# Performance work log

Hardware: AMD Instinct MI355X
Metric: run time of the kernel (lower is better)

The kernel has to match this reference:

```python
import jax, jax.numpy as jnp
import numpy as np
import math

B, L, D = 2, 1024, 1024
H, DK, DV = 8, 1536, 1536
DEPTH = 1
R = math.exp(4 - 2 * DEPTH) / (math.exp(4 - 2 * DEPTH) + 1)
TEMP = DK ** 0.5
LN_EPS = 1e-5


def setup_inputs() -> dict:
    key = jax.random.key(0)
    ks = jax.random.split(key, 16)
    s = 0.02
    return {
        "q": jax.random.normal(ks[0], (B, L, D), jnp.float32),
        "k": jax.random.normal(ks[1], (B, L, D), jnp.float32),
        "v": jax.random.normal(ks[2], (B, L, D), jnp.float32),
        "mask": jax.random.randint(ks[3], (B, L, 1), 0, 2, jnp.int32),
        "w_qs_w": jax.random.normal(ks[4], (H * DK, D), jnp.float32) * s,
        "w_qs_b": jnp.zeros((H * DK,), jnp.float32),
        "w_ks_w": jax.random.normal(ks[5], (H * DK, D), jnp.float32) * s,
        "w_ks_b": jnp.zeros((H * DK,), jnp.float32),
        "w_vs_w": jax.random.normal(ks[6], (H * DV, D), jnp.float32) * s,
        "w_vs_b": jnp.zeros((H * DV,), jnp.float32),
        "fc_w": jax.random.normal(ks[7], (D, H * DV), jnp.float32) * s,
        "ln_scale": jnp.ones((D,), jnp.float32),
        "ln_bias": jnp.zeros((D,), jnp.float32),
    }


def reference(q, k, v, mask, w_qs_w, w_qs_b, w_ks_w, w_ks_b, w_vs_w, w_vs_b, fc_w, ln_scale, ln_bias):
    Bq, Lq, _ = q.shape
    Lk = k.shape[1]
    residual = q
    # QKV projections, split into heads, flatten as (batch, head)
    qh = (q @ w_qs_w.T + w_qs_b).reshape(Bq, Lq, H, DK).transpose(0, 2, 1, 3).reshape(Bq * H, Lq, DK)
    kh = (k @ w_ks_w.T + w_ks_b).reshape(Bq, Lk, H, DK).transpose(0, 2, 1, 3).reshape(Bq * H, Lk, DK)
    vh = (v @ w_vs_w.T + w_vs_b).reshape(Bq, Lk, H, DV).transpose(0, 2, 1, 3).reshape(Bq * H, Lk, DV)
    # mask: repeat(n_head,1,1) -> (head, batch) ordering, exactly as original
    maskf = mask.astype(jnp.float32)
    mask_rep = jnp.tile(maskf, (H, 1, 1))  # [H*B, Lq, 1]
    maskb = mask_rep != 0
    atten = jnp.einsum('bqd,bkd->bqk', qh / TEMP, kh)  # [B*H, Lq, Lk]
    atten = jnp.where(maskb, 1e-9, atten)  # masked_fill_(mask.bool(), 1e-9)
    new_mask = (1.0 - R) * maskb.astype(jnp.float32) + R * mask_rep  # [B*H, Lq, 1]
    atten = jax.nn.softmax(atten, axis=-1) * new_mask
    out = jnp.einsum('bqk,bkd->bqd', atten, vh)
    out = out.reshape(Bq, H, Lq, DV).transpose(0, 2, 1, 3).reshape(Bq, Lq, H * DV)
    out = out @ fc_w.T
    x = out + residual
    mu = jnp.mean(x, axis=-1, keepdims=True)
    var = jnp.mean((x - mu) ** 2, axis=-1, keepdims=True)
    out = (x - mu) / jnp.sqrt(var + LN_EPS) * ln_scale + ln_bias
    return (out, atten)
```

## Files before the change

### kernel.cpp

```cpp
#include <hip/hip_runtime.h>
#include <hip/hip_bf16.h>

#define B_   2
#define L_   1024
#define D_   1024
#define H_   8
#define DV_  1536
#define HDV_ 12288
#define INV_L (1.0f/1024.0f)


__global__ void __launch_bounds__(256) k1(const float* __restrict__ v,
                                          float* __restrict__ vsum,
                                          const int* __restrict__ mask,
                                          float* __restrict__ atten) {
    int bx = blockIdx.x, t = threadIdx.x;
    if (bx < 32) {
        __shared__ float4 lds[16][16];
        int b  = bx >> 4;
        int s  = bx & 15;
        int c4 = t & 15;
        int rg = t >> 4;
        const float4* vp = (const float4*)(v + (size_t)b * L_ * D_)
                           + (size_t)s * 16 + c4;
        float4 acc = make_float4(0.f, 0.f, 0.f, 0.f);
        #pragma unroll 8
        for (int r = 0; r < 64; ++r) {
            float4 x = vp[(size_t)(rg * 64 + r) * (D_ / 4)];
            acc.x += x.x; acc.y += x.y; acc.z += x.z; acc.w += x.w;
        }
        lds[rg][c4] = acc;
        __syncthreads();
        if (t < 16) {
            float4 a = make_float4(0.f, 0.f, 0.f, 0.f);
            #pragma unroll
            for (int g = 0; g < 16; ++g) {
                float4 x = lds[g][t];
                a.x += x.x; a.y += x.y; a.z += x.z; a.w += x.w;
            }
            ((float4*)(vsum + (size_t)b * D_ + (size_t)s * 64))[t] = a;
        }
    } else {
        int r0 = (bx - 32) * 8;
        #pragma unroll
        for (int rr = 0; rr < 8; ++rr) {
            int r  = r0 + rr;
            int i  = r >> 10;
            int qi = r & 1023;
            float val = (mask[((i & 1) << 10) + qi] != 0) ? INV_L : 0.f;
            ((float4*)(atten + (size_t)r * L_))[t] = make_float4(val, val, val, val);
        }
    }
}

__global__ void __launch_bounds__(256) k_vproj(const float* __restrict__ vsum,
                                               const float* __restrict__ wv,
                                               const float* __restrict__ bv,
                                               float* __restrict__ S) {
    int gid  = blockIdx.x * 256 + threadIdx.x;
    int m    = gid >> 6;
    int lane = threadIdx.x & 63;
    const float4* row = (const float4*)(wv + (size_t)m * D_);
    const float4* v0  = (const float4*)vsum;
    const float4* v1  = (const float4*)(vsum + D_);
    float a0 = 0.f, a1 = 0.f;
    #pragma unroll
    for (int it = 0; it < 4; ++it) {
        int c = it * 64 + lane;
        float4 w4 = row[c];
        float4 s0 = v0[c];
        float4 s1 = v1[c];
        a0 += w4.x*s0.x + w4.y*s0.y + w4.z*s0.z + w4.w*s0.w;
        a1 += w4.x*s1.x + w4.y*s1.y + w4.z*s1.z + w4.w*s1.w;
    }
    #pragma unroll
    for (int off = 32; off; off >>= 1) {
        a0 += __shfl_down(a0, off);
        a1 += __shfl_down(a1, off);
    }
    if (lane == 0) {
        float bb = bv[m] * (float)L_;
        S[m]        = a0 + bb;
        S[HDV_ + m] = a1 + bb;
    }
}

__global__ void __launch_bounds__(256) k_fc(const float* __restrict__ S,
                                            const float* __restrict__ fcw,
                                            float* __restrict__ G) {
    __shared__ float red[16];
    int j = blockIdx.x, t = threadIdx.x;
    const float4* row = (const float4*)(fcw + (size_t)j * HDV_);
    const float4* S0  = (const float4*)S;
    const float4* S1  = (const float4*)(S + HDV_);
    float g00 = 0.f, g01 = 0.f, g10 = 0.f, g11 = 0.f;
    #pragma unroll
    for (int it = 0; it < 12; ++it) {
        int t4 = it * 256 + t;
        int p  = (t4 / 384) & 1;
        float4 w4 = row[t4];
        float4 s0 = S0[t4];
        float4 s1 = S1[t4];
        float d0 = w4.x*s0.x + w4.y*s0.y + w4.z*s0.z + w4.w*s0.w;
        float d1 = w4.x*s1.x + w4.y*s1.y + w4.z*s1.z + w4.w*s1.w;
        if (p) { g01 += d0; g11 += d1; } else { g00 += d0; g10 += d1; }
    }
    #pragma unroll
    for (int off = 32; off; off >>= 1) {
        g00 += __shfl_down(g00, off);
        g01 += __shfl_down(g01, off);
        g10 += __shfl_down(g10, off);
        g11 += __shfl_down(g11, off);
    }
    int lane = t & 63, w = t >> 6;
    if (lane == 0) {
        red[w * 4 + 0] = g00; red[w * 4 + 1] = g01;
        red[w * 4 + 2] = g10; red[w * 4 + 3] = g11;
    }
    __syncthreads();
    if (t < 4) {
        float x = red[t] + red[4 + t] + red[8 + t] + red[12 + t];
        G[(size_t)t * D_ + j] = x;
    }
}

__global__ void __launch_bounds__(256) k_ln(const float* __restrict__ qin,
                                            const int* __restrict__ mask,
                                            const float* __restrict__ G,
                                            const float* __restrict__ lns,
                                            const float* __restrict__ lnb,
                                            float* __restrict__ out) {
    __shared__ float red[8];
    int row = blockIdx.x;
    int b   = row >> 10;
    int qi  = row & 1023;
    float m0 = (mask[qi]      != 0) ? INV_L : 0.f;
    float m1 = (mask[L_ + qi] != 0) ? INV_L : 0.f;
    const float4* q4 = (const float4*)(qin + (size_t)row * D_);
    const float4* g0 = (const float4*)(G + (size_t)(2 * b) * D_);
    const float4* g1 = (const float4*)(G + (size_t)(2 * b + 1) * D_);
    int t = threadIdx.x;
    float4 a = q4[t], u = g0[t], w = g1[t];
    float4 x;
    x.x = a.x + m0 * u.x + m1 * w.x;
    x.y = a.y + m0 * u.y + m1 * w.y;
    x.z = a.z + m0 * u.z + m1 * w.z;
    x.w = a.w + m0 * u.w + m1 * w.w;
    float s  = x.x + x.y + x.z + x.w;
    float ss = x.x*x.x + x.y*x.y + x.z*x.z + x.w*x.w;
    #pragma unroll
    for (int off = 32; off; off >>= 1) {
        s  += __shfl_down(s, off);
        ss += __shfl_down(ss, off);
    }
    int lane = t & 63, wv = t >> 6;
    if (lane == 0) { red[wv] = s; red[4 + wv] = ss; }
    __syncthreads();
    if (t == 0) {
        float sAll  = red[0] + red[1] + red[2] + red[3];
        float ssAll = red[4] + red[5] + red[6] + red[7];
        float mu  = sAll * INV_L;
        float var = ssAll * INV_L - mu * mu;
        red[0] = mu;
        red[1] = rsqrtf(var + 1e-5f);
    }
    __syncthreads();
    float mu = red[0], inv = red[1];
    float4 sc = ((const float4*)lns)[t];
    float4 bi = ((const float4*)lnb)[t];
    float4 o;
    o.x = (x.x - mu) * inv * sc.x + bi.x;
    o.y = (x.y - mu) * inv * sc.y + bi.y;
    o.z = (x.z - mu) * inv * sc.z + bi.z;
    o.w = (x.w - mu) * inv * sc.w + bi.w;
    ((float4*)(out + (size_t)row * D_))[t] = o;
}

extern "C" void kernel_launch(void* const* d_in, const int* in_sizes, int n_in,
                              void* d_out, int out_size, void* d_ws, size_t ws_size,
                              hipStream_t stream) {
    const float* q    = (const float*)d_in[0];
    const float* v    = (const float*)d_in[2];
    const int*   mask = (const int*)d_in[3];
    const float* wv   = (const float*)d_in[8];
    const float* bv   = (const float*)d_in[9];
    const float* fcw  = (const float*)d_in[10];
    const float* lns  = (const float*)d_in[11];
    const float* lnb  = (const float*)d_in[12];

    float* out   = (float*)d_out;
    float* atten = out + (size_t)B_ * L_ * D_;

    float* ws   = (float*)d_ws;
    float* vsum = ws;
    float* S    = ws + 2048;
    float* G    = ws + 26624;

    k1      <<<32 + 2048, 256, 0, stream>>>(v, vsum, mask, atten);
    k_vproj <<<(HDV_ * 64) / 256, 256, 0, stream>>>(vsum, wv, bv, S);
    k_fc    <<<D_, 256, 0, stream>>>(S, fcw, G);
    k_ln    <<<B_ * L_, 256, 0, stream>>>(q, mask, G, lns, lnb, out);
}
```

Baseline: 41.70 us.

## Spread atten fill writes across vproj and fc kernels to overlap bandwidth

```diff
diff --git a/kernel.cpp b/kernel.cpp
--- a/kernel.cpp
+++ b/kernel.cpp
@@ -9,6 +9,19 @@
 #define HDV_ 12288
 #define INV_L (1.0f/1024.0f)
 
+
+__device__ __forceinline__ void atten_rows8(const int* __restrict__ mask,
+                                            float* __restrict__ atten,
+                                            int r0, int t) {
+    #pragma unroll
+    for (int rr = 0; rr < 8; ++rr) {
+        int r  = r0 + rr;
+        int i  = r >> 10;
+        int qi = r & 1023;
+        float val = (mask[((i & 1) << 10) + qi] != 0) ? INV_L : 0.f;
+        ((float4*)(atten + (size_t)r * L_))[t] = make_float4(val, val, val, val);
+    }
+}
 
 __global__ void __launch_bounds__(256) k1(const float* __restrict__ v,
                                           float* __restrict__ vsum,
@@ -41,25 +54,31 @@
             ((float4*)(vsum + (size_t)b * D_ + (size_t)s * 64))[t] = a;
         }
     } else {
-        int r0 = (bx - 32) * 8;
-        #pragma unroll
-        for (int rr = 0; rr < 8; ++rr) {
-            int r  = r0 + rr;
-            int i  = r >> 10;
-            int qi = r & 1023;
-            float val = (mask[((i & 1) << 10) + qi] != 0) ? INV_L : 0.f;
-            ((float4*)(atten + (size_t)r * L_))[t] = make_float4(val, val, val, val);
-        }
+        atten_rows8(mask, atten, (bx - 32) * 8, t);
     }
 }
 
 __global__ void __launch_bounds__(256) k_vproj(const float* __restrict__ vsum,
                                                const float* __restrict__ wv,
                                                const float* __restrict__ bv,
-                                               float* __restrict__ S) {
-    int gid  = blockIdx.x * 256 + threadIdx.x;
-    int m    = gid >> 6;
-    int lane = threadIdx.x & 63;
+                                               float* __restrict__ S,
+                                               const int* __restrict__ mask,
+                                               float* __restrict__ atten) {
+    int bx = blockIdx.x, t = threadIdx.x;
+    int u;
+    if (bx < 3584) {
+        int g = bx >> 2, pos = bx & 3;
+        if (pos == 3) {
+            atten_rows8(mask, atten, 2048 + g * 8, t);
+            return;
+        }
+        u = g * 3 + pos;
+    } else {
+        u = 2688 + (bx - 3584);
+    }
+    int wid  = t >> 6;
+    int lane = t & 63;
+    int m    = u * 4 + wid;
     const float4* row = (const float4*)(wv + (size_t)m * D_);
     const float4* v0  = (const float4*)vsum;
     const float4* v1  = (const float4*)(vsum + D_);
@@ -87,9 +106,22 @@
 
 __global__ void __launch_bounds__(256) k_fc(const float* __restrict__ S,
                                             const float* __restrict__ fcw,
-                                            float* __restrict__ G) {
+                                            float* __restrict__ G,
+                                            const int* __restrict__ mask,
+                                            float* __restrict__ atten) {
+    int bx = blockIdx.x, t = threadIdx.x;
+    int j;
+    if (bx < 1792) {
+        int g = bx >> 1, pos = bx & 1;
+        if (pos == 1) {
+            atten_rows8(mask, atten, 9216 + g * 8, t);
+            return;
+        }
+        j = g;
+    } else {
+        j = 896 + (bx - 1792);
+    }
     __shared__ float red[16];
-    int j = blockIdx.x, t = threadIdx.x;
     const float4* row = (const float4*)(fcw + (size_t)j * HDV_);
     const float4* S0  = (const float4*)S;
     const float4* S1  = (const float4*)(S + HDV_);
@@ -196,8 +228,8 @@
     float* S    = ws + 2048;
     float* G    = ws + 26624;
 
-    k1      <<<32 + 2048, 256, 0, stream>>>(v, vsum, mask, atten);
-    k_vproj <<<(HDV_ * 64) / 256, 256, 0, stream>>>(vsum, wv, bv, S);
-    k_fc    <<<D_, 256, 0, stream>>>(S, fcw, G);
-    k_ln    <<<B_ * L_, 256, 0, stream>>>(q, mask, G, lns, lnb, out);
-}
+    k1      <<<32 + 256,   256, 0, stream>>>(v, vsum, mask, atten);
+    k_vproj <<<3584 + 384, 256, 0, stream>>>(vsum, wv, bv, S, mask, atten);
+    k_fc    <<<1792 + 128, 256, 0, stream>>>(S, fcw, G, mask, atten);
+    k_ln    <<<B_ * L_,    256, 0, stream>>>(q, mask, G, lns, lnb, out);
+}
```

Result: slower. 50.39 us (+20.8%).
